# Performance work log

Measured on AMD Instinct MI355X. Metric: run time of the kernel, lower is better.

Reference implementation:

```python
import jax, jax.numpy as jnp
import numpy as np

EMBED_DIM = 1024
NUM_HEADS = 16
HEAD_DIM = EMBED_DIM // NUM_HEADS
LN_EPS = 1e-5


def setup_inputs() -> dict:
    key = jax.random.key(0)
    ks = jax.random.split(key, 6)
    b, s, d = 2, 2048, EMBED_DIM
    scale = 1.0 / np.sqrt(d)
    x = jax.random.normal(ks[0], (b, s, d), dtype=jnp.float32)
    w_qkv = jax.random.normal(ks[1], (d, 3 * d), dtype=jnp.float32) * scale
    b_qkv = jax.random.normal(ks[2], (3 * d,), dtype=jnp.float32) * 0.02
    w_out = jax.random.normal(ks[3], (d, d), dtype=jnp.float32) * scale
    b_out = jax.random.normal(ks[4], (d,), dtype=jnp.float32) * 0.02
    gamma = jnp.ones((d,), dtype=jnp.float32)
    ln_beta = jnp.zeros((d,), dtype=jnp.float32)
    beta = jax.random.normal(ks[5], (), dtype=jnp.float32) * 0.1
    return {"x": x, "w_qkv": w_qkv, "b_qkv": b_qkv, "w_out": w_out,
            "b_out": b_out, "gamma": gamma, "ln_beta": ln_beta, "beta": beta}


def _layernorm(x, gamma, ln_beta):
    mu = jnp.mean(x, axis=-1, keepdims=True)
    var = jnp.mean(jnp.square(x - mu), axis=-1, keepdims=True)
    return (x - mu) * jax.lax.rsqrt(var + LN_EPS) * gamma + ln_beta


def reference(x, w_qkv, b_qkv, w_out, b_out, gamma, ln_beta, beta):
    b, s, d = x.shape
    h, hd = NUM_HEADS, HEAD_DIM
    residual = x
    xn = _layernorm(x, gamma, ln_beta)
    qkv = xn @ w_qkv + b_qkv                       # [b, s, 3d]
    qkv = qkv.reshape(b, s, 3, h, hd)
    q = jnp.transpose(qkv[:, :, 0], (0, 2, 1, 3))  # [b, h, s, hd]
    k = jnp.transpose(qkv[:, :, 1], (0, 2, 1, 3))
    v = jnp.transpose(qkv[:, :, 2], (0, 2, 1, 3))
    attn = jnp.einsum('bhqd,bhkd->bhqk', q, k) / np.sqrt(hd)
    idx = jnp.arange(s)
    dist = jnp.abs(idx[None, :] - idx[:, None]).astype(attn.dtype)  # [s, s]
    attn = attn + beta * jnp.log1p(dist)[None, None, :, :]
    probs = jax.nn.softmax(attn, axis=-1)
    ctx = jnp.einsum('bhqk,bhkd->bhqd', probs, v)  # [b, h, s, hd]
    ctx = jnp.transpose(ctx, (0, 2, 1, 3)).reshape(b, s, d)
    return residual + ctx @ w_out + b_out
```

## Files before the change

kernel.cpp:

```cpp
#include <hip/hip_runtime.h>

#define SEQ 2048
#define DIM 1024
#define NHEAD 16
#define HDIM 64
#define NTOK 4096
#define N3D 3072

typedef __attribute__((ext_vector_type(8))) short bf16x8;
typedef __attribute__((ext_vector_type(4))) float floatx4;
typedef __attribute__((ext_vector_type(4))) unsigned short ushortx4;

__device__ __forceinline__ unsigned short f2bf(float f) {
    unsigned int u = __builtin_bit_cast(unsigned int, f);
    u += 0x7FFFu + ((u >> 16) & 1u);
    return (unsigned short)(u >> 16);
}

__device__ __forceinline__ void async_copy16(const void* g, const void* l) {
    __builtin_amdgcn_global_load_lds(
        (const __attribute__((address_space(1))) unsigned int*)(unsigned long long)g,
        (__attribute__((address_space(3))) unsigned int*)(unsigned int)(unsigned long long)l,
        16, 0, 0);
}

#define MFMA_BF16(a, b, c) __builtin_amdgcn_mfma_f32_16x16x32_bf16((a), (b), (c), 0, 0, 0)

__global__ __launch_bounds__(256)
void prep_kernel(const float* __restrict__ w_qkv, unsigned short* __restrict__ wqkvT,
                 const float* __restrict__ w_out, unsigned short* __restrict__ woutT,
                 const float* __restrict__ x, const float* __restrict__ gamma,
                 const float* __restrict__ lnb, unsigned short* __restrict__ xn) {
    const int bid = blockIdx.x;
    const int tid = threadIdx.x;
    if (bid < 4096) {
        __shared__ float tile[32][33];
        const float* src; unsigned short* dst; int cols, bx, by;
        if (bid < 3072) { src = w_qkv; dst = wqkvT; cols = N3D; bx = bid % 96; by = bid / 96; }
        else { int t = bid - 3072; src = w_out; dst = woutT; cols = DIM; bx = t & 31; by = t >> 5; }
        const int c0 = bx * 32, r0 = by * 32;
        const int tx = tid & 31, ty = tid >> 5;
        for (int i = 0; i < 4; ++i) {
            int r = ty + i * 8;
            tile[r][tx] = src[(size_t)(r0 + r) * cols + c0 + tx];
        }
        __syncthreads();
        for (int i = 0; i < 4; ++i) {
            int rr = ty + i * 8;
            dst[(size_t)(c0 + rr) * DIM + r0 + tx] = f2bf(tile[tx][rr]);
        }
    } else {
        const int row = bid - 4096;
        const float* xr = x + (size_t)row * DIM;
        float4 v = ((const float4*)xr)[tid];
        float s = v.x + v.y + v.z + v.w;
        float s2 = v.x * v.x + v.y * v.y + v.z * v.z + v.w * v.w;
        for (int off = 1; off < 64; off <<= 1) {
            s += __shfl_xor(s, off, 64);
            s2 += __shfl_xor(s2, off, 64);
        }
        __shared__ float red[8];
        const int wave = tid >> 6, lane = tid & 63;
        if (lane == 0) { red[wave] = s; red[4 + wave] = s2; }
        __syncthreads();
        s = red[0] + red[1] + red[2] + red[3];
        s2 = red[4] + red[5] + red[6] + red[7];
        const float mu = s * (1.0f / DIM);
        const float var = s2 * (1.0f / DIM) - mu * mu;
        const float rstd = rsqrtf(var + 1e-5f);
        float4 g = ((const float4*)gamma)[tid];
        float4 bb = ((const float4*)lnb)[tid];
        unsigned short* o = xn + (size_t)row * DIM + tid * 4;
        o[0] = f2bf((v.x - mu) * rstd * g.x + bb.x);
        o[1] = f2bf((v.y - mu) * rstd * g.y + bb.y);
        o[2] = f2bf((v.z - mu) * rstd * g.z + bb.z);
        o[3] = f2bf((v.w - mu) * rstd * g.w + bb.w);
    }
}

__global__ __launch_bounds__(256)
void qkv_gemm(const unsigned short* __restrict__ A, const unsigned short* __restrict__ Bt,
              const float* __restrict__ bias, unsigned short* __restrict__ qo,
              unsigned short* __restrict__ ko, unsigned short* __restrict__ vTo) {
    __shared__ unsigned short Asm[128 * 64];
    __shared__ unsigned short Bsm[192 * 64];
    const int tid = threadIdx.x;
    const int wave = tid >> 6, lane = tid & 63;
    const int quad = lane >> 4, r16 = lane & 15;
    const int flat = blockIdx.x;
    const int xcd = flat & 7, c = flat >> 3;
    const int mt = (xcd >> 1) * 8 + (c >> 3);
    const int nt = (xcd & 1) * 8 + (c & 7);
    const int m0 = mt * 128, n0 = nt * 192;
    const int wm = (wave & 1) * 64, wn = (wave >> 1) * 96;
    floatx4 acc[4][6] = {};
    for (int k0 = 0; k0 < DIM; k0 += 64) {
        __syncthreads();
        for (int p = 0; p < 4; ++p) {
            int s = tid + p * 256;
            int r = s >> 3, c8 = (s & 7) << 3;
            async_copy16(A + (size_t)(m0 + r) * DIM + k0 + c8, Asm + s * 8);
        }
        for (int p = 0; p < 6; ++p) {
            int s = tid + p * 256;
            int r = s >> 3, c8 = (s & 7) << 3;
            async_copy16(Bt + (size_t)(n0 + r) * DIM + k0 + c8, Bsm + s * 8);
        }
        __syncthreads();
        for (int h = 0; h < 2; ++h) {
            bf16x8 af[4], bfr[6];
            for (int i = 0; i < 4; ++i)
                af[i] = *(const bf16x8*)(Asm + (wm + i * 16 + r16) * 64 + h * 32 + quad * 8);
            for (int j = 0; j < 6; ++j)
                bfr[j] = *(const bf16x8*)(Bsm + (wn + j * 16 + r16) * 64 + h * 32 + quad * 8);
            for (int i = 0; i < 4; ++i)
                for (int j = 0; j < 6; ++j)
                    acc[i][j] = MFMA_BF16(af[i], bfr[j], acc[i][j]);
        }
    }
    for (int j = 0; j < 6; ++j) {
        int n = n0 + wn + j * 16 + r16;
        float bn = bias[n];
        int part = n >> 10, nn = n & 1023;
        int head = nn >> 6, hdi = nn & 63;
        for (int i = 0; i < 4; ++i) {
            int mbase = m0 + wm + i * 16 + quad * 4;
            int bIdx = mbase >> 11, sIdx = mbase & 2047;
            if (part == 2) {
                ushortx4 pack;
                for (int e = 0; e < 4; ++e) pack[e] = f2bf(acc[i][j][e] + bn);
                *(ushortx4*)(vTo + ((size_t)(bIdx * NHEAD + head) * HDIM + hdi) * SEQ + sIdx) = pack;
            } else {
                unsigned short* dst = (part == 0) ? qo : ko;
                for (int e = 0; e < 4; ++e)
                    dst[((size_t)(bIdx * NHEAD + head) * SEQ + sIdx + e) * HDIM + hdi] =
                        f2bf(acc[i][j][e] + bn);
            }
        }
    }
}

__global__ __launch_bounds__(512)
void attn_kernel(const unsigned short* __restrict__ qg, const unsigned short* __restrict__ kg,
                 const unsigned short* __restrict__ vTg, const float* __restrict__ betap,
                 unsigned short* __restrict__ ctx) {
    __shared__ unsigned short QP[128][72];
    __shared__ unsigned short Kd[2][64 * 64];
    __shared__ unsigned short Vd[2][64 * 64];
    __shared__ float logt[SEQ];

    const int tid = threadIdx.x;
    const int wave = tid >> 6, lane = tid & 63;
    const int quad = lane >> 4, r16 = lane & 15;
    const int flat = blockIdx.y * 16 + blockIdx.x;
    const int swz = (flat & 7) * 64 + (flat >> 3);
    const int bh = swz >> 4, qt = swz & 15;
    const int qBase = qt * 128;
    const float betaV = betap[0];
    const float L2E = 1.44269504f;
    const float c1 = 0.125f * L2E;

    for (int i = tid; i < SEQ; i += 512)
        logt[i] = betaV * log1pf((float)i) * L2E - 20.0f;

    const unsigned short* qptr = qg + ((size_t)bh * SEQ + qBase) * HDIM;
    for (int s = tid; s < 1024; s += 512) {
        int r = s >> 3, c8 = (s & 7) << 3;
        *(bf16x8*)(&QP[r][c8]) = *(const bf16x8*)(qptr + r * HDIM + c8);
    }

    const int sr = tid >> 3;
    const int scg = (tid & 7) ^ (sr & 7);
    const unsigned short* kbh = kg + (size_t)bh * SEQ * HDIM;
    const unsigned short* vbh = vTg + (size_t)bh * HDIM * SEQ;
    async_copy16(kbh + (size_t)sr * HDIM + scg * 8, &Kd[0][tid * 8]);
    async_copy16(vbh + (size_t)sr * SEQ + scg * 8, &Vd[0][tid * 8]);
    __syncthreads();

    bf16x8 qf0 = *(const bf16x8*)(&QP[wave * 16 + r16][quad * 8]);
    bf16x8 qf1 = *(const bf16x8*)(&QP[wave * 16 + r16][32 + quad * 8]);

    const bf16x8 onesv = {0x3F80, 0x3F80, 0x3F80, 0x3F80, 0x3F80, 0x3F80, 0x3F80, 0x3F80};

    floatx4 o[5] = {};
    const int qWaveBase = qBase + wave * 16;
    const int qrT = qWaveBase + r16;

    for (int kt0 = 0; kt0 < SEQ; kt0 += 64) {
        const int buf = (kt0 >> 6) & 1;
        if (kt0 + 64 < SEQ) {
            async_copy16(kbh + (size_t)(kt0 + 64 + sr) * HDIM + scg * 8, &Kd[buf ^ 1][tid * 8]);
            async_copy16(vbh + (size_t)sr * SEQ + kt0 + 64 + scg * 8, &Vd[buf ^ 1][tid * 8]);
        }

        floatx4 sc[4];
        __builtin_amdgcn_s_setprio(1);
        for (int ct = 0; ct < 4; ++ct) {
            int rK = ct * 16 + r16;
            const unsigned short* kb = &Kd[buf][rK * 64];
            bf16x8 kf0 = *(const bf16x8*)(kb + ((quad ^ (rK & 7)) << 3));
            bf16x8 kf1 = *(const bf16x8*)(kb + (((quad ^ 4) ^ (rK & 7)) << 3));
            floatx4 z = {0.f, 0.f, 0.f, 0.f};
            z = MFMA_BF16(kf0, qf0, z);
            z = MFMA_BF16(kf1, qf1, z);
            sc[ct] = z;
        }
        __builtin_amdgcn_s_setprio(0);
        for (int ct = 0; ct < 4; ++ct) {
            const int keyTile = kt0 + ct * 16;
            const int kbase = keyTile + quad * 4;
            if (qWaveBase >= keyTile + 16) {
                const float* lp = &logt[qrT - kbase - 3];
                for (int i = 0; i < 4; ++i)
                    sc[ct][i] = __builtin_amdgcn_exp2f(sc[ct][i] * c1 + lp[3 - i]);
            } else if (keyTile >= qWaveBase + 16) {
                const float* lp = &logt[kbase - qrT];
                for (int i = 0; i < 4; ++i)
                    sc[ct][i] = __builtin_amdgcn_exp2f(sc[ct][i] * c1 + lp[i]);
            } else {
                for (int i = 0; i < 4; ++i) {
                    int dist = qrT - (kbase + i);
                    dist = dist < 0 ? -dist : dist;
                    sc[ct][i] = __builtin_amdgcn_exp2f(sc[ct][i] * c1 + logt[dist]);
                }
            }
        }
        {
            unsigned short* prow = &QP[wave * 16 + r16][0];
            for (int ct = 0; ct < 4; ++ct) {
                unsigned int lo, hi;
                asm("v_cvt_pk_bf16_f32 %0, %1, %2" : "=v"(lo) : "v"(sc[ct][0]), "v"(sc[ct][1]));
                asm("v_cvt_pk_bf16_f32 %0, %1, %2" : "=v"(hi) : "v"(sc[ct][2]), "v"(sc[ct][3]));
                uint2 pk; pk.x = lo; pk.y = hi;
                *(uint2*)(prow + ct * 16 + quad * 4) = pk;
            }
        }
        bf16x8 pf0 = *(const bf16x8*)(&QP[wave * 16 + r16][quad * 8]);
        bf16x8 pf1 = *(const bf16x8*)(&QP[wave * 16 + r16][32 + quad * 8]);
        __builtin_amdgcn_s_setprio(1);
        for (int nt = 0; nt < 4; ++nt) {
            int rV = nt * 16 + r16;
            const unsigned short* vb = &Vd[buf][rV * 64];
            bf16x8 vf0 = *(const bf16x8*)(vb + ((quad ^ (rV & 7)) << 3));
            bf16x8 vf1 = *(const bf16x8*)(vb + (((quad ^ 4) ^ (rV & 7)) << 3));
            o[nt] = MFMA_BF16(pf0, vf0, o[nt]);
            o[nt] = MFMA_BF16(pf1, vf1, o[nt]);
        }
        o[4] = MFMA_BF16(pf0, onesv, o[4]);
        o[4] = MFMA_BF16(pf1, onesv, o[4]);
        __builtin_amdgcn_s_setprio(0);

        __syncthreads();
    }

    const int b_ = bh >> 4, h_ = bh & 15;
    for (int i = 0; i < 4; ++i) {
        float inv = 1.0f / o[4][i];
        int qi = qBase + wave * 16 + quad * 4 + i;
        for (int nt = 0; nt < 4; ++nt) {
            int d = nt * 16 + r16;
            ctx[((size_t)(b_ * SEQ + qi)) * DIM + h_ * HDIM + d] = f2bf(o[nt][i] * inv);
        }
    }
}

__global__ __launch_bounds__(256)
void out_gemm(const unsigned short* __restrict__ A, const unsigned short* __restrict__ Bt,
              const float* __restrict__ bias, const float* __restrict__ resid,
              float* __restrict__ out) {
    __shared__ unsigned short Asm[128 * 64];
    __shared__ unsigned short Bsm[64 * 64];
    const int tid = threadIdx.x;
    const int wave = tid >> 6, lane = tid & 63;
    const int quad = lane >> 4, r16 = lane & 15;
    const int flat = blockIdx.y * 16 + blockIdx.x;
    const int swz = (flat & 7) * 64 + (flat >> 3);
    const int m0 = (swz >> 4) * 128, n0 = (swz & 15) * 64;
    const int wm = (wave & 1) * 64, wn = (wave >> 1) * 32;
    floatx4 acc[4][2] = {};
    for (int k0 = 0; k0 < DIM; k0 += 64) {
        __syncthreads();
        for (int p = 0; p < 4; ++p) {
            int s = tid + p * 256;
            int r = s >> 3, c8 = (s & 7) << 3;
            async_copy16(A + (size_t)(m0 + r) * DIM + k0 + c8, Asm + s * 8);
        }
        for (int p = 0; p < 2; ++p) {
            int s = tid + p * 256;
            int r = s >> 3, c8 = (s & 7) << 3;
            async_copy16(Bt + (size_t)(n0 + r) * DIM + k0 + c8, Bsm + s * 8);
        }
        __syncthreads();
        for (int h = 0; h < 2; ++h) {
            bf16x8 af[4], bfr[2];
            for (int i = 0; i < 4; ++i)
                af[i] = *(const bf16x8*)(Asm + (wm + i * 16 + r16) * 64 + h * 32 + quad * 8);
            for (int j = 0; j < 2; ++j)
                bfr[j] = *(const bf16x8*)(Bsm + (wn + j * 16 + r16) * 64 + h * 32 + quad * 8);
            for (int i = 0; i < 4; ++i)
                for (int j = 0; j < 2; ++j)
                    acc[i][j] = MFMA_BF16(af[i], bfr[j], acc[i][j]);
        }
    }
    for (int i = 0; i < 4; ++i)
        for (int j = 0; j < 2; ++j)
            for (int e = 0; e < 4; ++e) {
                int m = m0 + wm + i * 16 + quad * 4 + e;
                int n = n0 + wn + j * 16 + r16;
                out[(size_t)m * DIM + n] = acc[i][j][e] + bias[n] + resid[(size_t)m * DIM + n];
            }
}

extern "C" void kernel_launch(void* const* d_in, const int* in_sizes, int n_in,
                              void* d_out, int out_size, void* d_ws, size_t ws_size,
                              hipStream_t stream) {
    const float* x     = (const float*)d_in[0];
    const float* w_qkv = (const float*)d_in[1];
    const float* b_qkv = (const float*)d_in[2];
    const float* w_out = (const float*)d_in[3];
    const float* b_out = (const float*)d_in[4];
    const float* gamma = (const float*)d_in[5];
    const float* ln_b  = (const float*)d_in[6];
    const float* beta  = (const float*)d_in[7];
    float* out = (float*)d_out;

    char* ws = (char*)d_ws;
    const size_t MB = 1u << 20;
    unsigned short* xn    = (unsigned short*)(ws);
    unsigned short* wqkvT = (unsigned short*)(ws + 8 * MB);
    unsigned short* woutT = (unsigned short*)(ws + 14 * MB);
    unsigned short* qb    = (unsigned short*)(ws + 16 * MB);
    unsigned short* kb    = (unsigned short*)(ws + 24 * MB);
    unsigned short* vTb   = (unsigned short*)(ws + 32 * MB);
    unsigned short* ctx   = xn;

    prep_kernel<<<8192, 256, 0, stream>>>(w_qkv, wqkvT, w_out, woutT, x, gamma, ln_b, xn);
    qkv_gemm<<<512, 256, 0, stream>>>(xn, wqkvT, b_qkv, qb, kb, vTb);
    attn_kernel<<<dim3(SEQ / 128, 32), 512, 0, stream>>>(qb, kb, vTb, beta, ctx);
    out_gemm<<<dim3(16, 32), 256, 0, stream>>>(ctx, woutT, b_out, x, out);
}
```

Baseline: 234.1 us.

## Double-buffer LDS tiles in QKV and output GEMMs to overlap loads with MFMA

Both GEMM kernels now keep two LDS stages. Each iteration issues the async global-to-LDS copies for the next K tile before running the MFMAs on the current one, and ends with a single barrier instead of two. The aim is to hide global memory latency behind compute. This doubles LDS use per block, which may lower occupancy (the QKV kernel goes to about 80KB). Correctness relies on the barrier after compute also covering completion of the async copies.

```diff
diff --git a/kernel.cpp b/kernel.cpp
--- a/kernel.cpp
+++ b/kernel.cpp
@@ -82,8 +82,8 @@
 void qkv_gemm(const unsigned short* __restrict__ A, const unsigned short* __restrict__ Bt,
               const float* __restrict__ bias, unsigned short* __restrict__ qo,
               unsigned short* __restrict__ ko, unsigned short* __restrict__ vTo) {
-    __shared__ unsigned short Asm[128 * 64];
-    __shared__ unsigned short Bsm[192 * 64];
+    __shared__ unsigned short Asm[2][128 * 64];
+    __shared__ unsigned short Bsm[2][192 * 64];
     const int tid = threadIdx.x;
     const int wave = tid >> 6, lane = tid & 63;
     const int quad = lane >> 4, r16 = lane & 15;
@@ -93,31 +93,45 @@
     const int nt = (xcd & 1) * 8 + (c & 7);
     const int m0 = mt * 128, n0 = nt * 192;
     const int wm = (wave & 1) * 64, wn = (wave >> 1) * 96;
+    const int srA = tid >> 3, scA = (tid & 7) << 3;
     floatx4 acc[4][6] = {};
-    for (int k0 = 0; k0 < DIM; k0 += 64) {
-        __syncthreads();
-        for (int p = 0; p < 4; ++p) {
-            int s = tid + p * 256;
-            int r = s >> 3, c8 = (s & 7) << 3;
-            async_copy16(A + (size_t)(m0 + r) * DIM + k0 + c8, Asm + s * 8);
-        }
-        for (int p = 0; p < 6; ++p) {
-            int s = tid + p * 256;
-            int r = s >> 3, c8 = (s & 7) << 3;
-            async_copy16(Bt + (size_t)(n0 + r) * DIM + k0 + c8, Bsm + s * 8);
-        }
-        __syncthreads();
+    for (int p = 0; p < 4; ++p) {
+        int s = tid + p * 256;
+        async_copy16(A + (size_t)(m0 + (s >> 3)) * DIM + ((s & 7) << 3), &Asm[0][s * 8]);
+    }
+    for (int p = 0; p < 6; ++p) {
+        int s = tid + p * 256;
+        async_copy16(Bt + (size_t)(n0 + (s >> 3)) * DIM + ((s & 7) << 3), &Bsm[0][s * 8]);
+    }
+    __syncthreads();
+    for (int it = 0; it < 16; ++it) {
+        const int cur = it & 1;
+        if (it + 1 < 16) {
+            const int k1 = (it + 1) * 64;
+            for (int p = 0; p < 4; ++p) {
+                int s = tid + p * 256;
+                async_copy16(A + (size_t)(m0 + (s >> 3)) * DIM + k1 + ((s & 7) << 3),
+                             &Asm[cur ^ 1][s * 8]);
+            }
+            for (int p = 0; p < 6; ++p) {
+                int s = tid + p * 256;
+                async_copy16(Bt + (size_t)(n0 + (s >> 3)) * DIM + k1 + ((s & 7) << 3),
+                             &Bsm[cur ^ 1][s * 8]);
+            }
+        }
         for (int h = 0; h < 2; ++h) {
             bf16x8 af[4], bfr[6];
             for (int i = 0; i < 4; ++i)
-                af[i] = *(const bf16x8*)(Asm + (wm + i * 16 + r16) * 64 + h * 32 + quad * 8);
+                af[i] = *(const bf16x8*)(&Asm[cur][(wm + i * 16 + r16) * 64 + h * 32 + quad * 8]);
             for (int j = 0; j < 6; ++j)
-                bfr[j] = *(const bf16x8*)(Bsm + (wn + j * 16 + r16) * 64 + h * 32 + quad * 8);
+                bfr[j] = *(const bf16x8*)(&Bsm[cur][(wn + j * 16 + r16) * 64 + h * 32 + quad * 8]);
             for (int i = 0; i < 4; ++i)
                 for (int j = 0; j < 6; ++j)
                     acc[i][j] = MFMA_BF16(af[i], bfr[j], acc[i][j]);
         }
-    }
+        __syncthreads();
+    }
+    (void)srA; (void)scA;
     for (int j = 0; j < 6; ++j) {
         int n = n0 + wn + j * 16 + r16;
         float bn = bias[n];
@@ -268,8 +282,8 @@
 void out_gemm(const unsigned short* __restrict__ A, const unsigned short* __restrict__ Bt,
               const float* __restrict__ bias, const float* __restrict__ resid,
               float* __restrict__ out) {
-    __shared__ unsigned short Asm[128 * 64];
-    __shared__ unsigned short Bsm[64 * 64];
+    __shared__ unsigned short Asm[2][128 * 64];
+    __shared__ unsigned short Bsm[2][64 * 64];
     const int tid = threadIdx.x;
     const int wave = tid >> 6, lane = tid & 63;
     const int quad = lane >> 4, r16 = lane & 15;
@@ -278,29 +292,41 @@
     const int m0 = (swz >> 4) * 128, n0 = (swz & 15) * 64;
     const int wm = (wave & 1) * 64, wn = (wave >> 1) * 32;
     floatx4 acc[4][2] = {};
-    for (int k0 = 0; k0 < DIM; k0 += 64) {
-        __syncthreads();
-        for (int p = 0; p < 4; ++p) {
-            int s = tid + p * 256;
-            int r = s >> 3, c8 = (s & 7) << 3;
-            async_copy16(A + (size_t)(m0 + r) * DIM + k0 + c8, Asm + s * 8);
-        }
-        for (int p = 0; p < 2; ++p) {
-            int s = tid + p * 256;
-            int r = s >> 3, c8 = (s & 7) << 3;
-            async_copy16(Bt + (size_t)(n0 + r) * DIM + k0 + c8, Bsm + s * 8);
-        }
-        __syncthreads();
+    for (int p = 0; p < 4; ++p) {
+        int s = tid + p * 256;
+        async_copy16(A + (size_t)(m0 + (s >> 3)) * DIM + ((s & 7) << 3), &Asm[0][s * 8]);
+    }
+    for (int p = 0; p < 2; ++p) {
+        int s = tid + p * 256;
+        async_copy16(Bt + (size_t)(n0 + (s >> 3)) * DIM + ((s & 7) << 3), &Bsm[0][s * 8]);
+    }
+    __syncthreads();
+    for (int it = 0; it < 16; ++it) {
+        const int cur = it & 1;
+        if (it + 1 < 16) {
+            const int k1 = (it + 1) * 64;
+            for (int p = 0; p < 4; ++p) {
+                int s = tid + p * 256;
+                async_copy16(A + (size_t)(m0 + (s >> 3)) * DIM + k1 + ((s & 7) << 3),
+                             &Asm[cur ^ 1][s * 8]);
+            }
+            for (int p = 0; p < 2; ++p) {
+                int s = tid + p * 256;
+                async_copy16(Bt + (size_t)(n0 + (s >> 3)) * DIM + k1 + ((s & 7) << 3),
+                             &Bsm[cur ^ 1][s * 8]);
+            }
+        }
         for (int h = 0; h < 2; ++h) {
             bf16x8 af[4], bfr[2];
             for (int i = 0; i < 4; ++i)
-                af[i] = *(const bf16x8*)(Asm + (wm + i * 16 + r16) * 64 + h * 32 + quad * 8);
+                af[i] = *(const bf16x8*)(&Asm[cur][(wm + i * 16 + r16) * 64 + h * 32 + quad * 8]);
             for (int j = 0; j < 2; ++j)
-                bfr[j] = *(const bf16x8*)(Bsm + (wn + j * 16 + r16) * 64 + h * 32 + quad * 8);
+                bfr[j] = *(const bf16x8*)(&Bsm[cur][(wn + j * 16 + r16) * 64 + h * 32 + quad * 8]);
             for (int i = 0; i < 4; ++i)
                 for (int j = 0; j < 2; ++j)
                     acc[i][j] = MFMA_BF16(af[i], bfr[j], acc[i][j]);
         }
+        __syncthreads();
     }
     for (int i = 0; i < 4; ++i)
         for (int j = 0; j < 2; ++j)
```

Result: faster. 216.8 us (-7.4%).

## Retile QKV GEMM to 128x128 tiles and double-buffer output GEMM loads

Applied to the files above, without the earlier changes.

The QKV projection GEMM moves from 128x192 tiles on 512 blocks to 128x128 tiles on 768 blocks, with a new XCD-aware block-to-tile mapping. This gives more blocks and fewer registers per thread in exchange for less reuse of each A tile. The output-projection GEMM now double-buffers its shared-memory A/B tiles, prefetching the next K slice while computing the current one and using one barrier per iteration. This is meant to hide global-to-LDS latency, at the cost of twice the LDS footprint.

```diff
diff --git a/kernel.cpp b/kernel.cpp
--- a/kernel.cpp
+++ b/kernel.cpp
@@ -83,42 +83,38 @@
               const float* __restrict__ bias, unsigned short* __restrict__ qo,
               unsigned short* __restrict__ ko, unsigned short* __restrict__ vTo) {
     __shared__ unsigned short Asm[128 * 64];
-    __shared__ unsigned short Bsm[192 * 64];
+    __shared__ unsigned short Bsm[128 * 64];
     const int tid = threadIdx.x;
     const int wave = tid >> 6, lane = tid & 63;
     const int quad = lane >> 4, r16 = lane & 15;
     const int flat = blockIdx.x;
     const int xcd = flat & 7, c = flat >> 3;
-    const int mt = (xcd >> 1) * 8 + (c >> 3);
-    const int nt = (xcd & 1) * 8 + (c & 7);
-    const int m0 = mt * 128, n0 = nt * 192;
-    const int wm = (wave & 1) * 64, wn = (wave >> 1) * 96;
-    floatx4 acc[4][6] = {};
+    const int mt = xcd * 4 + c / 24;
+    const int nt = c % 24;
+    const int m0 = mt * 128, n0 = nt * 128;
+    const int wm = (wave & 1) * 64, wn = (wave >> 1) * 64;
+    floatx4 acc[4][4] = {};
     for (int k0 = 0; k0 < DIM; k0 += 64) {
         __syncthreads();
         for (int p = 0; p < 4; ++p) {
             int s = tid + p * 256;
             int r = s >> 3, c8 = (s & 7) << 3;
             async_copy16(A + (size_t)(m0 + r) * DIM + k0 + c8, Asm + s * 8);
-        }
-        for (int p = 0; p < 6; ++p) {
-            int s = tid + p * 256;
-            int r = s >> 3, c8 = (s & 7) << 3;
             async_copy16(Bt + (size_t)(n0 + r) * DIM + k0 + c8, Bsm + s * 8);
         }
         __syncthreads();
         for (int h = 0; h < 2; ++h) {
-            bf16x8 af[4], bfr[6];
+            bf16x8 af[4], bfr[4];
             for (int i = 0; i < 4; ++i)
                 af[i] = *(const bf16x8*)(Asm + (wm + i * 16 + r16) * 64 + h * 32 + quad * 8);
-            for (int j = 0; j < 6; ++j)
+            for (int j = 0; j < 4; ++j)
                 bfr[j] = *(const bf16x8*)(Bsm + (wn + j * 16 + r16) * 64 + h * 32 + quad * 8);
             for (int i = 0; i < 4; ++i)
-                for (int j = 0; j < 6; ++j)
+                for (int j = 0; j < 4; ++j)
                     acc[i][j] = MFMA_BF16(af[i], bfr[j], acc[i][j]);
         }
     }
-    for (int j = 0; j < 6; ++j) {
+    for (int j = 0; j < 4; ++j) {
         int n = n0 + wn + j * 16 + r16;
         float bn = bias[n];
         int part = n >> 10, nn = n & 1023;
@@ -268,8 +264,8 @@
 void out_gemm(const unsigned short* __restrict__ A, const unsigned short* __restrict__ Bt,
               const float* __restrict__ bias, const float* __restrict__ resid,
               float* __restrict__ out) {
-    __shared__ unsigned short Asm[128 * 64];
-    __shared__ unsigned short Bsm[64 * 64];
+    __shared__ unsigned short Asm[2][128 * 64];
+    __shared__ unsigned short Bsm[2][64 * 64];
     const int tid = threadIdx.x;
     const int wave = tid >> 6, lane = tid & 63;
     const int quad = lane >> 4, r16 = lane & 15;
@@ -278,29 +274,41 @@
     const int m0 = (swz >> 4) * 128, n0 = (swz & 15) * 64;
     const int wm = (wave & 1) * 64, wn = (wave >> 1) * 32;
     floatx4 acc[4][2] = {};
-    for (int k0 = 0; k0 < DIM; k0 += 64) {
-        __syncthreads();
-        for (int p = 0; p < 4; ++p) {
-            int s = tid + p * 256;
-            int r = s >> 3, c8 = (s & 7) << 3;
-            async_copy16(A + (size_t)(m0 + r) * DIM + k0 + c8, Asm + s * 8);
-        }
-        for (int p = 0; p < 2; ++p) {
-            int s = tid + p * 256;
-            int r = s >> 3, c8 = (s & 7) << 3;
-            async_copy16(Bt + (size_t)(n0 + r) * DIM + k0 + c8, Bsm + s * 8);
-        }
-        __syncthreads();
+    for (int p = 0; p < 4; ++p) {
+        int s = tid + p * 256;
+        async_copy16(A + (size_t)(m0 + (s >> 3)) * DIM + ((s & 7) << 3), &Asm[0][s * 8]);
+    }
+    for (int p = 0; p < 2; ++p) {
+        int s = tid + p * 256;
+        async_copy16(Bt + (size_t)(n0 + (s >> 3)) * DIM + ((s & 7) << 3), &Bsm[0][s * 8]);
+    }
+    __syncthreads();
+    for (int it = 0; it < 16; ++it) {
+        const int cur = it & 1;
+        if (it + 1 < 16) {
+            const int k1 = (it + 1) * 64;
+            for (int p = 0; p < 4; ++p) {
+                int s = tid + p * 256;
+                async_copy16(A + (size_t)(m0 + (s >> 3)) * DIM + k1 + ((s & 7) << 3),
+                             &Asm[cur ^ 1][s * 8]);
+            }
+            for (int p = 0; p < 2; ++p) {
+                int s = tid + p * 256;
+                async_copy16(Bt + (size_t)(n0 + (s >> 3)) * DIM + k1 + ((s & 7) << 3),
+                             &Bsm[cur ^ 1][s * 8]);
+            }
+        }
         for (int h = 0; h < 2; ++h) {
             bf16x8 af[4], bfr[2];
             for (int i = 0; i < 4; ++i)
-                af[i] = *(const bf16x8*)(Asm + (wm + i * 16 + r16) * 64 + h * 32 + quad * 8);
+                af[i] = *(const bf16x8*)(&Asm[cur][(wm + i * 16 + r16) * 64 + h * 32 + quad * 8]);
             for (int j = 0; j < 2; ++j)
-                bfr[j] = *(const bf16x8*)(Bsm + (wn + j * 16 + r16) * 64 + h * 32 + quad * 8);
+                bfr[j] = *(const bf16x8*)(&Bsm[cur][(wn + j * 16 + r16) * 64 + h * 32 + quad * 8]);
             for (int i = 0; i < 4; ++i)
                 for (int j = 0; j < 2; ++j)
                     acc[i][j] = MFMA_BF16(af[i], bfr[j], acc[i][j]);
         }
+        __syncthreads();
     }
     for (int i = 0; i < 4; ++i)
         for (int j = 0; j < 2; ++j)
@@ -335,7 +343,7 @@
     unsigned short* ctx   = xn;
 
     prep_kernel<<<8192, 256, 0, stream>>>(w_qkv, wqkvT, w_out, woutT, x, gamma, ln_b, xn);
-    qkv_gemm<<<512, 256, 0, stream>>>(xn, wqkvT, b_qkv, qb, kb, vTb);
+    qkv_gemm<<<768, 256, 0, stream>>>(xn, wqkvT, b_qkv, qb, kb, vTb);
     attn_kernel<<<dim3(SEQ / 128, 32), 512, 0, stream>>>(qb, kb, vTb, beta, ctx);
     out_gemm<<<dim3(16, 32), 256, 0, stream>>>(ctx, woutT, b_out, x, out);
 }
```

Result: faster. 222.3 us (-5.0%).
